# Kernel optimization log

Hardware: AMD Instinct MI355X
Metric: run time of the kernel (lower is better)

Reference implementation:

```python
import jax, jax.numpy as jnp
import numpy as np

N0, N1, N2, N3, B = 120000, 20000, 6000, 1600, 64
E1, E2, E3 = 480000, 144000, 38400
KS = 5  # kernel size per dim; K = 125 total


def spline_basis(pseudo, ks=KS):
    # open B-spline basis, degree 1, over [0,1]^3 (torch_spline_conv semantics)
    p = pseudo * (ks - 1)                       # (E,3)
    lo = jnp.clip(jnp.floor(p), 0.0, ks - 2.0)  # (E,3)
    f = p - lo                                  # fractional part
    bits = jnp.array([[(s >> d) & 1 for d in range(3)] for s in range(8)],
                     dtype=jnp.float32)         # (8,3) corner offsets
    w = jnp.where(bits[None] > 0, f[:, None, :], 1.0 - f[:, None, :])  # (E,8,3)
    basis = w[..., 0] * w[..., 1] * w[..., 2]   # (E,8)
    strides = jnp.array([1.0, ks, ks * ks], dtype=jnp.float32)
    kidx = ((lo[:, None, :] + bits[None]) * strides).sum(-1).astype(jnp.int32)  # (E,8)
    return basis, kidx


def spline_conv(x, edge_index, pseudo, W, root, bias, num_nodes):
    src, dst = edge_index[0], edge_index[1]
    basis, kidx = spline_basis(pseudo)                   # (E,8), (E,8)
    XW = jnp.einsum('ni,kio->nko', x, W)                 # (N,K,out)
    taps = XW[src[:, None], kidx]                        # (E,8,out) gather
    msg = (taps * basis[..., None]).sum(axis=1)          # (E,out)
    agg = jax.ops.segment_sum(msg, dst, num_segments=num_nodes)
    deg = jax.ops.segment_sum(jnp.ones_like(dst, jnp.float32), dst,
                              num_segments=num_nodes)
    agg = agg / jnp.maximum(deg, 1.0)[:, None]           # mean aggregation
    return agg + x @ root + bias


def seg_max(x, seg, n):
    v = jax.ops.segment_max(x, seg, num_segments=n)
    return jnp.where(jnp.isfinite(v), v, 0.0)  # empty voxels -> 0


def setup_inputs() -> dict:
    key = jax.random.key(0)
    ks = jax.random.split(key, 24)
    return {
        'x0': jax.random.uniform(ks[0], (N0, 1), jnp.float32),
        'cluster0': jax.random.randint(ks[1], (N0,), 0, N1),
        'edge1': jax.random.randint(ks[2], (2, E1), 0, N1),
        'pseudo1': jax.random.uniform(ks[3], (E1, 3), jnp.float32),
        'W1': jax.random.normal(ks[4], (125, 1, 64), jnp.float32) * 0.1,
        'root1': jax.random.normal(ks[5], (1, 64), jnp.float32) * 0.1,
        'b1': jnp.zeros((64,), jnp.float32),
        'cluster1': jax.random.randint(ks[6], (N1,), 0, N2),
        'edge2': jax.random.randint(ks[7], (2, E2), 0, N2),
        'pseudo2': jax.random.uniform(ks[8], (E2, 3), jnp.float32),
        'W2': jax.random.normal(ks[9], (125, 64, 64), jnp.float32) * 0.05,
        'root2': jax.random.normal(ks[10], (64, 64), jnp.float32) * 0.05,
        'b2': jnp.zeros((64,), jnp.float32),
        'cluster2': jax.random.randint(ks[11], (N2,), 0, N3),
        'edge3': jax.random.randint(ks[12], (2, E3), 0, N3),
        'pseudo3': jax.random.uniform(ks[13], (E3, 3), jnp.float32),
        'W3': jax.random.normal(ks[14], (125, 64, 128), jnp.float32) * 0.05,
        'root3': jax.random.normal(ks[15], (64, 128), jnp.float32) * 0.05,
        'b3': jnp.zeros((128,), jnp.float32),
        'cluster3': jax.random.randint(ks[16], (N3,), 0, B * 8),
        'fc1_w': jax.random.normal(ks[17], (1024, 256), jnp.float32) * 0.03,
        'fc1_b': jnp.zeros((256,), jnp.float32),
        'fc2_w': jax.random.normal(ks[18], (256, 10), jnp.float32) * 0.06,
        'fc2_b': jnp.zeros((10,), jnp.float32),
    }


def reference(x0, cluster0, edge1, pseudo1, W1, root1, b1,
              cluster1, edge2, pseudo2, W2, root2, b2,
              cluster2, edge3, pseudo3, W3, root3, b3,
              cluster3, fc1_w, fc1_b, fc2_w, fc2_b):
    x = seg_max(x0, cluster0, N1)                       # sparse voxel max pool 1
    x = jax.nn.elu(spline_conv(x, edge1, pseudo1, W1, root1, b1, N1))
    x = seg_max(x, cluster1, N2)                        # pool 2
    x = jax.nn.elu(spline_conv(x, edge2, pseudo2, W2, root2, b2, N2))
    x = seg_max(x, cluster2, N3)                        # pool 3
    x = jax.nn.elu(spline_conv(x, edge3, pseudo3, W3, root3, b3, N3))
    x = seg_max(x, cluster3, B * 8)                     # dense 2x2x2 voxel pool
    x = x.reshape(B, 8 * 128)
    x = jax.nn.elu(x @ fc1_w + fc1_b)
    x = x @ fc2_w + fc2_b
    return jax.nn.log_softmax(x, axis=1)
```

## Files before the change

### kernel.cpp

```cpp
#include <hip/hip_runtime.h>
#include <hip/hip_bf16.h>
#include <math.h>

#define N0c 120000
#define N1c 20000
#define N2c 6000
#define N3c 1600
#define E1c 480000
#define E2c 144000
#define E3c 38400

#define HB1 32
#define HB2 120
#define HB3 40
#define CVT2B 2000
#define CVT3B 4000
#define SS0B  469

typedef __attribute__((ext_vector_type(8))) short short8;
typedef __attribute__((ext_vector_type(4))) float f32x4;

__device__ __forceinline__ float eluf(float x) {
    return x > 0.0f ? x : expm1f(x);
}

__device__ __forceinline__ unsigned f2sort(float f) {
    unsigned u = __float_as_uint(f);
    return (u & 0x80000000u) ? ~u : (u | 0x80000000u);
}
__device__ __forceinline__ float sort2f(unsigned u) {
    unsigned bits = (u & 0x80000000u) ? (u & 0x7FFFFFFFu) : ~u;
    return __uint_as_float(bits);
}
__device__ __forceinline__ unsigned short f2bf(float v) {
    unsigned u = __float_as_uint(v);
    unsigned r = (u + 0x7FFFu + ((u >> 16) & 1u)) >> 16;
    return (unsigned short)r;
}

__global__ __launch_bounds__(256) void hist_all(
    const int* __restrict__ edge1, const int* __restrict__ edge2,
    const int* __restrict__ edge3,
    const float* __restrict__ pseudo2, const float* __restrict__ pseudo3,
    const float* __restrict__ W2, const float* __restrict__ W3,
    const float* __restrict__ x0, const int* __restrict__ cluster0,
    int* __restrict__ blockCnt1,
    int* __restrict__ blockCnt2, int* __restrict__ cntD2,
    int* __restrict__ blockCnt3, int* __restrict__ cntD3,
    unsigned short* __restrict__ W2t, unsigned short* __restrict__ W3t,
    unsigned* __restrict__ xm1)
{
    __shared__ int h[1250];
    int b = blockIdx.x, t = threadIdx.x;
    if (b < HB1) {
        for (int i = t; i < 1250; i += 256) h[i] = 0;
        __syncthreads();
        for (int e = b * 256 + t; e < E1c; e += HB1 * 256)
            atomicAdd(&h[edge1[E1c + e] >> 4], 1);
        __syncthreads();
        for (int i = t; i < 1250; i += 256) blockCnt1[i * HB1 + b] = h[i];
    } else if (b < HB1 + HB2 + HB3) {
        bool is2 = b < HB1 + HB2;
        int rb = is2 ? (b - HB1) : (b - HB1 - HB2);
        int nblk = is2 ? HB2 : HB3;
        int E = is2 ? E2c : E3c;
        const int* edge = is2 ? edge2 : edge3;
        const float* pseudo = is2 ? pseudo2 : pseudo3;
        int* blockCnt = is2 ? blockCnt2 : blockCnt3;
        int* dstCnt = is2 ? cntD2 : cntD3;
        int nb = is2 ? HB2 : HB3;
        if (t < 64) h[t] = 0;
        __syncthreads();
        for (int e = rb * 256 + t; e < E; e += nblk * 256) {
            int c = 0, mul = 1;
            #pragma unroll
            for (int d = 0; d < 3; d++) {
                float p = pseudo[e * 3 + d] * 4.0f;
                float l = fminf(fmaxf(floorf(p), 0.0f), 3.0f);
                c += (int)l * mul;
                mul <<= 2;
            }
            atomicAdd(&h[c], 1);
            atomicAdd(&dstCnt[edge[E + e]], 1);
        }
        __syncthreads();
        if (t < 64) blockCnt[t * nb + rb] = h[t];
    } else if (b < HB1 + HB2 + HB3 + CVT2B) {
        int idx = (b - (HB1 + HB2 + HB3)) * 256 + t;
        if (idx < 125 * 64 * 64) {
            int ic = idx & 63, kn = idx >> 6;
            int n = kn & 63, k = kn >> 6;
            W2t[idx] = f2bf(W2[((size_t)k * 64 + ic) * 64 + n]);
        }
    } else if (b < HB1 + HB2 + HB3 + CVT2B + CVT3B) {
        int idx = (b - (HB1 + HB2 + HB3 + CVT2B)) * 256 + t;
        if (idx < 125 * 128 * 64) {
            int ic = idx & 63, kn = idx >> 6;
            int n = kn & 127, k = kn >> 7;
            W3t[idx] = f2bf(W3[((size_t)k * 64 + ic) * 128 + n]);
        }
    } else {
        int idx = (b - (HB1 + HB2 + HB3 + CVT2B + CVT3B)) * 256 + t;
        if (idx < N0c)
            atomicMax(&xm1[cluster0[idx]], f2sort(x0[idx]));
    }
}

__global__ __launch_bounds__(256) void plan_tot(
    const int* __restrict__ blockCnt1, int* __restrict__ start1,
    const int* __restrict__ blockCnt2, int* __restrict__ binCnt2,
    int* __restrict__ binStart2, int* __restrict__ blkPrefix2,
    int* __restrict__ chunkBin2, int* __restrict__ chunkOff2,
    const int* __restrict__ blockCnt3, int* __restrict__ binCnt3,
    int* __restrict__ binStart3, int* __restrict__ blkPrefix3,
    int* __restrict__ chunkBin3, int* __restrict__ chunkOff3)
{
    __shared__ int ps[256];
    __shared__ int ps64[64];
    int t = threadIdx.x;

    int loc[5];
    int s = 0;
    #pragma unroll
    for (int i = 0; i < 5; i++) {
        int bin = t * 5 + i;
        int v = 0;
        if (bin < 1250) {
            const int4* row = (const int4*)(blockCnt1 + (size_t)bin * HB1);
            #pragma unroll
            for (int j = 0; j < HB1 / 4; j++) {
                int4 q = row[j];
                v += q.x + q.y + q.z + q.w;
            }
        }
        loc[i] = v;
        s += v;
    }
    ps[t] = s;
    __syncthreads();
    for (int ofs = 1; ofs < 256; ofs <<= 1) {
        int add = (t >= ofs) ? ps[t - ofs] : 0;
        __syncthreads();
        ps[t] += add;
        __syncthreads();
    }
    int run = (t == 0) ? 0 : ps[t - 1];
    #pragma unroll
    for (int i = 0; i < 5; i++) {
        int bin = t * 5 + i;
        if (bin < 1250) {
            start1[bin] = run;
            run += loc[i];
        }
    }
    if (t == 255) start1[1250] = run;
    __syncthreads();

    if (t < 64) {
        int v = 0;
        const int4* row = (const int4*)(blockCnt2 + (size_t)t * HB2);
        for (int j = 0; j < HB2 / 4; j++) {
            int4 q = row[j];
            v += q.x + q.y + q.z + q.w;
        }
        binCnt2[t] = v;
        ps64[t] = v;
    }
    __syncthreads();
    if (t == 0) {
        int s2 = 0, p = 0;
        for (int c = 0; c < 64; c++) {
            int v = ps64[c];
            binStart2[c] = s2;
            blkPrefix2[c] = p;
            s2 += v;
            p += (v + 63) >> 6;
        }
        binStart2[64] = s2;
        blkPrefix2[64] = p;
    }
    __syncthreads();
    if (t < 64) {
        int nch = (binCnt2[t] + 63) >> 6;
        int base = blkPrefix2[t];
        for (int j = 0; j < nch; j++) {
            chunkBin2[base + j] = t;
            chunkOff2[base + j] = j;
        }
    }
    __syncthreads();

    if (t < 64) {
        int v = 0;
        const int4* row = (const int4*)(blockCnt3 + (size_t)t * HB3);
        for (int j = 0; j < HB3 / 4; j++) {
            int4 q = row[j];
            v += q.x + q.y + q.z + q.w;
        }
        binCnt3[t] = v;
        ps64[t] = v;
    }
    __syncthreads();
    if (t == 0) {
        int s3 = 0, p = 0;
        for (int c = 0; c < 64; c++) {
            int v = ps64[c];
            binStart3[c] = s3;
            blkPrefix3[c] = p;
            s3 += v;
            p += (v + 63) >> 6;
        }
        binStart3[64] = s3;
        blkPrefix3[64] = p;
    }
    __syncthreads();
    if (t < 64) {
        int nch = (binCnt3[t] + 63) >> 6;
        int base = blkPrefix3[t];
        for (int j = 0; j < nch; j++) {
            chunkBin3[base + j] = t;
            chunkOff3[base + j] = j;
        }
    }
}

__global__ __launch_bounds__(256) void off_all(
    const int* __restrict__ blockCnt1, const int* __restrict__ start1,
    int* __restrict__ blockOff1,
    const int* __restrict__ blockCnt2, const int* __restrict__ binStart2,
    int* __restrict__ blockOff2,
    const int* __restrict__ blockCnt3, const int* __restrict__ binStart3,
    int* __restrict__ blockOff3)
{
    int r = blockIdx.x * 256 + threadIdx.x;
    if (r < 1250) {
        int run = start1[r];
        const int* c = blockCnt1 + (size_t)r * HB1;
        int* o = blockOff1 + (size_t)r * HB1;
        #pragma unroll 4
        for (int b = 0; b < HB1; b++) { o[b] = run; run += c[b]; }
    } else if (r < 1250 + 64) {
        int bin = r - 1250;
        int run = binStart2[bin];
        const int* c = blockCnt2 + (size_t)bin * HB2;
        int* o = blockOff2 + (size_t)bin * HB2;
        #pragma unroll 4
        for (int b = 0; b < HB2; b++) { o[b] = run; run += c[b]; }
    } else if (r < 1250 + 128) {
        int bin = r - 1314;
        int run = binStart3[bin];
        const int* c = blockCnt3 + (size_t)bin * HB3;
        int* o = blockOff3 + (size_t)bin * HB3;
        #pragma unroll 4
        for (int b = 0; b < HB3; b++) { o[b] = run; run += c[b]; }
    }
}

__global__ __launch_bounds__(256) void scatter_all(
    const int* __restrict__ edge1, const float* __restrict__ pseudo1,
    const int* __restrict__ edge2, const float* __restrict__ pseudo2,
    const int* __restrict__ edge3, const float* __restrict__ pseudo3,
    const int* __restrict__ blockOff1, const int* __restrict__ blockOff2,
    const int* __restrict__ blockOff3,
    int4* __restrict__ rec1, int4* __restrict__ rec2, int4* __restrict__ rec3,
    unsigned* __restrict__ xm1)
{
    __shared__ int cur[1250];
    int b = blockIdx.x, t = threadIdx.x;
    if (b < HB1) {
        for (int i = t; i < 1250; i += 256) cur[i] = blockOff1[(size_t)i * HB1 + b];
        __syncthreads();
        for (int e = b * 256 + t; e < E1c; e += HB1 * 256) {
            int src = edge1[e], dst = edge1[E1c + e];
            float f[3];
            int kbase = 0, mul5 = 1;
            #pragma unroll
            for (int d = 0; d < 3; d++) {
                float pp = pseudo1[e * 3 + d] * 4.0f;
                float l = fminf(fmaxf(floorf(pp), 0.0f), 3.0f);
                f[d] = pp - l;
                kbase += (int)l * mul5;
                mul5 *= 5;
            }
            int p = atomicAdd(&cur[dst >> 4], 1);
            rec1[p] = make_int4(src | ((dst & 15) << 16) | (kbase << 20),
                                __float_as_int(f[0]), __float_as_int(f[1]),
                                __float_as_int(f[2]));
        }
    } else if (b < HB1 + HB2 + HB3) {
        bool is2 = b < HB1 + HB2;
        int rb = is2 ? (b - HB1) : (b - HB1 - HB2);
        int nblk = is2 ? HB2 : HB3;
        int E = is2 ? E2c : E3c;
        const int* edge = is2 ? edge2 : edge3;
        const float* pseudo = is2 ? pseudo2 : pseudo3;
        const int* blockOff = is2 ? blockOff2 : blockOff3;
        int4* rec = is2 ? rec2 : rec3;
        int nb = is2 ? HB2 : HB3;
        if (t < 64) cur[t] = blockOff[(size_t)t * nb + rb];
        __syncthreads();
        for (int e = rb * 256 + t; e < E; e += nblk * 256) {
            int src = edge[e], dst = edge[E + e];
            float f[3];
            int c = 0, mul = 1;
            #pragma unroll
            for (int d = 0; d < 3; d++) {
                float pp = pseudo[e * 3 + d] * 4.0f;
                float l = fminf(fmaxf(floorf(pp), 0.0f), 3.0f);
                f[d] = pp - l;
                c += (int)l * mul;
                mul <<= 2;
            }
            int p = atomicAdd(&cur[c], 1);
            rec[p] = make_int4(src | (dst << 16),
                               __float_as_int(f[0]), __float_as_int(f[1]),
                               __float_as_int(f[2]));
        }
    } else {
        int idx = (b - (HB1 + HB2 + HB3)) * 256 + t;
        if (idx < N1c) {
            float f = sort2f(xm1[idx]);
            unsigned bb = __float_as_uint(f);
            if ((bb & 0x7F800000u) == 0x7F800000u) f = 0.0f;
            ((float*)xm1)[idx] = f;
        }
    }
}

__global__ __launch_bounds__(256) void conv1_block(
    const int4* __restrict__ rec, const float* __restrict__ x,
    const int* __restrict__ start,
    const float* __restrict__ W, const float* __restrict__ root,
    const float* __restrict__ bias, const int* __restrict__ cl,
    unsigned* __restrict__ xmOut) {
    __shared__ float T[16][128];
    __shared__ int degL[16];
    int b = blockIdx.x;
    for (int j = threadIdx.x; j < 2048; j += 256) ((float*)T)[j] = 0.0f;
    if (threadIdx.x < 16) degL[threadIdx.x] = 0;
    __syncthreads();
    int s0 = start[b], s1 = start[b + 1];
    for (int i = s0 + threadIdx.x; i < s1; i += 256) {
        int4 r = rec[i];
        int src = r.x & 0xFFFF;
        int ln = (r.x >> 16) & 15;
        int kbase = r.x >> 20;
        float f0 = __int_as_float(r.y);
        float f1 = __int_as_float(r.z);
        float f2 = __int_as_float(r.w);
        float xv = x[src];
        #pragma unroll
        for (int s = 0; s < 8; s++) {
            int b0 = s & 1, b1 = (s >> 1) & 1, b2 = (s >> 2) & 1;
            float w0 = b0 ? f0 : 1.0f - f0;
            float w1 = b1 ? f1 : 1.0f - f1;
            float w2 = b2 ? f2 : 1.0f - f2;
            int k = kbase + b0 + 5 * b1 + 25 * b2;
            atomicAdd(&T[ln][k], xv * w0 * w1 * w2);
        }
        atomicAdd(&degL[ln], 1);
    }
    __syncthreads();
    int w = threadIdx.x >> 6, lane = threadIdx.x & 63;
    float acc[4] = {0.0f, 0.0f, 0.0f, 0.0f};
    for (int k = 0; k < 125; k++) {
        float wv = W[(k << 6) + lane];
        #pragma unroll
        for (int j = 0; j < 4; j++)
            acc[j] = fmaf(T[w + 4 * j][k], wv, acc[j]);
    }
    int v0 = b << 4;
    #pragma unroll
    for (int j = 0; j < 4; j++) {
        int ln = w + 4 * j;
        int v = v0 + ln;
        float d = fmaxf((float)degL[ln], 1.0f);
        float val = eluf(acc[j] / d + x[v] * root[lane] + bias[lane]);
        atomicMax(&xmOut[((size_t)cl[v] << 6) + lane], f2sort(val));
    }
}

__global__ void decode_cvt(unsigned* __restrict__ buf,
                           unsigned short* __restrict__ xb, int total) {
    int idx = blockIdx.x * blockDim.x + threadIdx.x;
    if (idx >= total) return;
    float f = sort2f(buf[idx]);
    unsigned b = __float_as_uint(f);
    if ((b & 0x7F800000u) == 0x7F800000u) f = 0.0f;
    ((float*)buf)[idx] = f;
    xb[idx] = f2bf(f);
}

__global__ void segmax_decode(unsigned* __restrict__ buf, int total) {
    int idx = blockIdx.x * blockDim.x + threadIdx.x;
    if (idx >= total) return;
    float f = sort2f(buf[idx]);
    unsigned b = __float_as_uint(f);
    if ((b & 0x7F800000u) == 0x7F800000u) f = 0.0f;
    ((float*)buf)[idx] = f;
}

template<int COUT>
__global__ __launch_bounds__(256) void spline_mfma(
    const int4* __restrict__ recs,
    const unsigned short* __restrict__ Wt,
    const unsigned short* __restrict__ xb,
    const int* __restrict__ binStart,
    const int* __restrict__ binCnt,
    const int* __restrict__ blkPrefix,
    const int* __restrict__ chunkBin,
    const int* __restrict__ chunkOff,
    float* __restrict__ agg)
{
    __shared__ float basisS[4][8][64];
    __shared__ int srcS[4][64];
    __shared__ int dstS[4][64];

    int w = threadIdx.x >> 6, lane = threadIdx.x & 63;
    int c = blockIdx.x * 4 + w;
    if (c >= blkPrefix[64]) return;
    int bin = chunkBin[c];
    int chunk = chunkOff[c];
    int cnt = binCnt[bin];

    {
        int pos = chunk * 64 + lane;
        bool act = pos < cnt;
        int4 r = act ? recs[binStart[bin] + pos] : make_int4(0, 0, 0, 0);
        srcS[w][lane] = r.x & 0xFFFF;
        dstS[w][lane] = act ? (r.x >> 16) : -1;
        float f0 = __int_as_float(r.y);
        float f1 = __int_as_float(r.z);
        float f2 = __int_as_float(r.w);
        #pragma unroll
        for (int s = 0; s < 8; s++) {
            float w0 = (s & 1) ? f0 : 1.0f - f0;
            float w1 = (s & 2) ? f1 : 1.0f - f1;
            float w2 = (s & 4) ? f2 : 1.0f - f2;
            basisS[w][s][lane] = act ? (w0 * w1 * w2) : 0.0f;
        }
    }
    __builtin_amdgcn_wave_barrier();
    __threadfence_block();

    int lo0 = bin & 3, lo1 = (bin >> 2) & 3, lo2 = bin >> 4;
    int kbase = lo0 + 5 * lo1 + 25 * lo2;
    int colOff = (COUT == 128) ? (blockIdx.y << 6) : 0;
    int q = lane >> 4;
    int mcol = lane & 15;

    short8 afr[4][2];
    #pragma unroll
    for (int rt = 0; rt < 4; rt++) {
        int src = srcS[w][rt * 16 + mcol];
        const unsigned short* xr = xb + ((size_t)src << 6) + q * 8;
        afr[rt][0] = *(const short8*)(xr);
        afr[rt][1] = *(const short8*)(xr + 32);
    }

    f32x4 acc[4][4];
    #pragma unroll
    for (int rt = 0; rt < 4; rt++)
        #pragma unroll
        for (int nt = 0; nt < 4; nt++)
            acc[rt][nt] = (f32x4){0.0f, 0.0f, 0.0f, 0.0f};
    const f32x4 zero4 = {0.0f, 0.0f, 0.0f, 0.0f};

    #pragma unroll 1
    for (int s = 0; s < 8; s++) {
        int k = kbase + (s & 1) + 5 * ((s >> 1) & 1) + 25 * (s >> 2);
        const unsigned short* Wk = Wt + ((size_t)k * COUT + colOff) * 64;
        short8 bfr[4][2];
        #pragma unroll
        for (int nt = 0; nt < 4; nt++) {
            const unsigned short* Wn = Wk + (size_t)(nt * 16 + mcol) * 64 + q * 8;
            bfr[nt][0] = *(const short8*)(Wn);
            bfr[nt][1] = *(const short8*)(Wn + 32);
        }
        #pragma unroll
        for (int rt = 0; rt < 4; rt++) {
            f32x4 ct[4];
            #pragma unroll
            for (int nt = 0; nt < 4; nt++) {
                ct[nt] = __builtin_amdgcn_mfma_f32_16x16x32_bf16(afr[rt][0], bfr[nt][0], zero4, 0, 0, 0);
                ct[nt] = __builtin_amdgcn_mfma_f32_16x16x32_bf16(afr[rt][1], bfr[nt][1], ct[nt], 0, 0, 0);
            }
            #pragma unroll
            for (int r = 0; r < 4; r++) {
                float bs = basisS[w][s][rt * 16 + q * 4 + r];
                #pragma unroll
                for (int nt = 0; nt < 4; nt++)
                    acc[rt][nt][r] = fmaf(bs, ct[nt][r], acc[rt][nt][r]);
            }
        }
    }

    #pragma unroll
    for (int rt = 0; rt < 4; rt++) {
        #pragma unroll
        for (int r = 0; r < 4; r++) {
            int d = dstS[w][rt * 16 + q * 4 + r];
            if (d >= 0) {
                float* ap = agg + (size_t)d * COUT + colOff + mcol;
                #pragma unroll
                for (int nt = 0; nt < 4; nt++)
                    atomicAdd(ap + nt * 16, acc[rt][nt][r]);
            }
        }
    }
}

__global__ __launch_bounds__(256) void node_update64(
    const float* __restrict__ agg, const int* __restrict__ deg,
    const float* __restrict__ xm, const float* __restrict__ root,
    const float* __restrict__ bias, const int* __restrict__ cl,
    unsigned* __restrict__ xmOut, int nNodes) {
    __shared__ float xsh[4][64];
    int w = threadIdx.x >> 6, lane = threadIdx.x & 63;
    int v = blockIdx.x * 4 + w;
    if (v >= nNodes) return;
    xsh[w][lane] = xm[((size_t)v << 6) + lane];
    float a = agg[((size_t)v << 6) + lane] / fmaxf((float)deg[v], 1.0f);
    float r = 0.0f;
    #pragma unroll 8
    for (int i = 0; i < 64; i++)
        r = fmaf(xsh[w][i], root[(i << 6) + lane], r);
    float val = eluf(a + r + bias[lane]);
    atomicMax(&xmOut[((size_t)cl[v] << 6) + lane], f2sort(val));
}

__global__ __launch_bounds__(256) void node_update128(
    const float* __restrict__ agg, const int* __restrict__ deg,
    const float* __restrict__ xm, const float* __restrict__ root,
    const float* __restrict__ bias, const int* __restrict__ cl,
    unsigned* __restrict__ xmOut, int nNodes) {
    __shared__ float xsh[4][64];
    int w = threadIdx.x >> 6, lane = threadIdx.x & 63;
    int v = blockIdx.x * 4 + w;
    if (v >= nNodes) return;
    xsh[w][lane] = xm[((size_t)v << 6) + lane];
    float dinv = 1.0f / fmaxf((float)deg[v], 1.0f);
    float a0 = agg[((size_t)v << 7) + lane] * dinv;
    float a1 = agg[((size_t)v << 7) + 64 + lane] * dinv;
    float r0 = 0.0f, r1 = 0.0f;
    #pragma unroll 8
    for (int i = 0; i < 64; i++) {
        float xi = xsh[w][i];
        r0 = fmaf(xi, root[(i << 7) + lane], r0);
        r1 = fmaf(xi, root[(i << 7) + 64 + lane], r1);
    }
    unsigned* orow = xmOut + ((size_t)cl[v] << 7);
    atomicMax(&orow[lane], f2sort(eluf(a0 + r0 + bias[lane])));
    atomicMax(&orow[64 + lane], f2sort(eluf(a1 + r1 + bias[lane + 64])));
}

__global__ __launch_bounds__(256) void fc1_split(
    const float* __restrict__ xin, const float* __restrict__ w1,
    float* __restrict__ h) {
    __shared__ float xsh[128];
    int row = blockIdx.x, ks = blockIdx.y;
    int o = threadIdx.x;
    if (o < 128) xsh[o] = xin[row * 1024 + ks * 128 + o];
    __syncthreads();
    float acc = 0.0f;
    const float* wp = w1 + (size_t)ks * 128 * 256 + o;
    #pragma unroll 8
    for (int i = 0; i < 128; i++)
        acc = fmaf(xsh[i], wp[i * 256], acc);
    atomicAdd(&h[row * 256 + o], acc);
}

__global__ __launch_bounds__(64) void fc2_k(
    const float* __restrict__ h, const float* __restrict__ b1,
    const float* __restrict__ w2, const float* __restrict__ b2,
    float* __restrict__ out) {
    __shared__ float hs[256];
    __shared__ float lg[10];
    int row = blockIdx.x;
    int t = threadIdx.x;
    for (int i = t; i < 256; i += 64) hs[i] = eluf(h[row * 256 + i] + b1[i]);
    __syncthreads();
    if (t < 10) {
        float a = b2[t];
        for (int i = 0; i < 256; i++) a = fmaf(hs[i], w2[i * 10 + t], a);
        lg[t] = a;
    }
    __syncthreads();
    if (t < 10) {
        float m = -1e30f;
        #pragma unroll
        for (int j = 0; j < 10; j++) m = fmaxf(m, lg[j]);
        float sum = 0.0f;
        #pragma unroll
        for (int j = 0; j < 10; j++) sum += expf(lg[j] - m);
        out[row * 10 + t] = lg[t] - m - logf(sum);
    }
}

extern "C" void kernel_launch(void* const* d_in, const int* in_sizes, int n_in,
                              void* d_out, int out_size, void* d_ws, size_t ws_size,
                              hipStream_t stream) {
    const float* x0      = (const float*)d_in[0];
    const int*   cluster0= (const int*)d_in[1];
    const int*   edge1   = (const int*)d_in[2];
    const float* pseudo1 = (const float*)d_in[3];
    const float* W1      = (const float*)d_in[4];
    const float* root1   = (const float*)d_in[5];
    const float* b1      = (const float*)d_in[6];
    const int*   cluster1= (const int*)d_in[7];
    const int*   edge2   = (const int*)d_in[8];
    const float* pseudo2 = (const float*)d_in[9];
    const float* W2      = (const float*)d_in[10];
    const float* root2   = (const float*)d_in[11];
    const float* b2      = (const float*)d_in[12];
    const int*   cluster2= (const int*)d_in[13];
    const int*   edge3   = (const int*)d_in[14];
    const float* pseudo3 = (const float*)d_in[15];
    const float* W3      = (const float*)d_in[16];
    const float* root3   = (const float*)d_in[17];
    const float* b3      = (const float*)d_in[18];
    const int*   cluster3= (const int*)d_in[19];
    const float* fc1_w   = (const float*)d_in[20];
    const float* fc1_b   = (const float*)d_in[21];
    const float* fc2_w   = (const float*)d_in[22];
    const float* fc2_b   = (const float*)d_in[23];
    float* out = (float*)d_out;

    float* ws = (float*)d_ws;
    size_t off = 0;
    float* xm1  = ws + off; off += 20480;
    float* xm2  = ws + off; off += (size_t)N2c * 64;
    float* xm3  = ws + off; off += (size_t)N3c * 64;
    float* xm4  = ws + off; off += 512 * 128;
    float* agg2 = ws + off; off += (size_t)N2c * 64;
    float* agg3 = ws + off; off += (size_t)N3c * 128;
    float* h1   = ws + off; off += 64 * 256;
    int* cntD2   = (int*)(ws + off); off += 6016;
    int* cntD3   = (int*)(ws + off); off += 1664;
    size_t zeroFloats = off;
    int4* rec1 = (int4*)(ws + off); off += (size_t)E1c * 4;
    int4* rec2 = (int4*)(ws + off); off += (size_t)E2c * 4;
    int4* rec3 = (int4*)(ws + off); off += (size_t)E3c * 4;
    unsigned short* W2t = (unsigned short*)(ws + off); off += 256000;
    unsigned short* W3t = (unsigned short*)(ws + off); off += 512000;
    unsigned short* xb2 = (unsigned short*)(ws + off); off += 192000;
    unsigned short* xb3 = (unsigned short*)(ws + off); off += 51200;
    int* start1    = (int*)(ws + off); off += 1280;
    int* blockCnt1 = (int*)(ws + off); off += HB1 * 1250;
    int* blockOff1 = (int*)(ws + off); off += HB1 * 1250;
    int* blockCnt2 = (int*)(ws + off); off += HB2 * 64;
    int* blockOff2 = (int*)(ws + off); off += HB2 * 64;
    int* blockCnt3 = (int*)(ws + off); off += HB3 * 64;
    int* blockOff3 = (int*)(ws + off); off += HB3 * 64;
    int* binCnt2   = (int*)(ws + off); off += 64;
    int* binStart2 = (int*)(ws + off); off += 80;
    int* blkPrefix2= (int*)(ws + off); off += 80;
    int* chunkBin2 = (int*)(ws + off); off += 2560;
    int* chunkOff2 = (int*)(ws + off); off += 2560;
    int* binCnt3   = (int*)(ws + off); off += 64;
    int* binStart3 = (int*)(ws + off); off += 80;
    int* blkPrefix3= (int*)(ws + off); off += 80;
    int* chunkBin3 = (int*)(ws + off); off += 768;
    int* chunkOff3 = (int*)(ws + off); off += 768;

    hipMemsetAsync(d_ws, 0, zeroFloats * sizeof(float), stream);

    hist_all<<<HB1 + HB2 + HB3 + CVT2B + CVT3B + SS0B, 256, 0, stream>>>(
        edge1, edge2, edge3, pseudo2, pseudo3, W2, W3, x0, cluster0,
        blockCnt1, blockCnt2, cntD2, blockCnt3, cntD3,
        W2t, W3t, (unsigned*)xm1);

    plan_tot<<<1, 256, 0, stream>>>(
        blockCnt1, start1,
        blockCnt2, binCnt2, binStart2, blkPrefix2, chunkBin2, chunkOff2,
        blockCnt3, binCnt3, binStart3, blkPrefix3, chunkBin3, chunkOff3);

    off_all<<<6, 256, 0, stream>>>(
        blockCnt1, start1, blockOff1,
        blockCnt2, binStart2, blockOff2,
        blockCnt3, binStart3, blockOff3);

    scatter_all<<<HB1 + HB2 + HB3 + (N1c + 255) / 256, 256, 0, stream>>>(
        edge1, pseudo1, edge2, pseudo2, edge3, pseudo3,
        blockOff1, blockOff2, blockOff3, rec1, rec2, rec3, (unsigned*)xm1);

    conv1_block<<<1250, 256, 0, stream>>>(rec1, xm1, start1, W1, root1, b1,
                                          cluster1, (unsigned*)xm2);
    decode_cvt<<<(N2c * 64) / 256, 256, 0, stream>>>((unsigned*)xm2, xb2, N2c * 64);

    spline_mfma<64><<<dim3((E2c / 64 + 64 + 3) / 4, 1), 256, 0, stream>>>(
        rec2, W2t, xb2, binStart2, binCnt2, blkPrefix2, chunkBin2, chunkOff2, agg2);
    node_update64<<<(N2c + 3) / 4, 256, 0, stream>>>(agg2, cntD2, xm2, root2, b2,
                                                     cluster2, (unsigned*)xm3, N2c);
    decode_cvt<<<(N3c * 64) / 256, 256, 0, stream>>>((unsigned*)xm3, xb3, N3c * 64);

    spline_mfma<128><<<dim3((E3c / 64 + 64 + 3) / 4, 2), 256, 0, stream>>>(
        rec3, W3t, xb3, binStart3, binCnt3, blkPrefix3, chunkBin3, chunkOff3, agg3);
    node_update128<<<(N3c + 3) / 4, 256, 0, stream>>>(agg3, cntD3, xm3, root3, b3,
                                                      cluster3, (unsigned*)xm4, N3c);
    segmax_decode<<<(512 * 128) / 256, 256, 0, stream>>>((unsigned*)xm4, 512 * 128);

    fc1_split<<<dim3(64, 8), 256, 0, stream>>>(xm4, fc1_w, h1);
    fc2_k<<<64, 64, 0, stream>>>(h1, fc1_b, fc2_w, fc2_b, out);
}
```

Baseline: 350.5 us.

## Replace atomic scatter-add aggregation with per-edge messages and CSR gather

Layers 2 and 3 of the spline conv no longer atomically add each edge message into a per-node accumulator. The MFMA kernel writes dense per-edge messages, and the scatter pass builds a destination-sorted position list using a prefix sum over degrees computed in plan_tot. The node update kernels then gather and sum each node's messages deterministically. This removes float atomics and the zeroing of the aggregation buffers, at the cost of a larger message buffer (E2 x 64 floats), extra scatter atomics and posList writes, random reads in the gather, and a serial scan added to the single-block plan kernel.

New measurement: 349.9 us. No clear change (-0.2%).

```diff
diff --git a/kernel.cpp b/kernel.cpp
--- a/kernel.cpp
+++ b/kernel.cpp
@@ -113,7 +113,9 @@
     int* __restrict__ chunkBin2, int* __restrict__ chunkOff2,
     const int* __restrict__ blockCnt3, int* __restrict__ binCnt3,
     int* __restrict__ binStart3, int* __restrict__ blkPrefix3,
-    int* __restrict__ chunkBin3, int* __restrict__ chunkOff3)
+    int* __restrict__ chunkBin3, int* __restrict__ chunkOff3,
+    const int* __restrict__ cntD2, int* __restrict__ dstStart2,
+    const int* __restrict__ cntD3, int* __restrict__ dstStart3)
 {
     __shared__ int ps[256];
     __shared__ int ps64[64];
@@ -221,6 +223,62 @@
             chunkBin3[base + j] = t;
             chunkOff3[base + j] = j;
         }
+    }
+    __syncthreads();
+
+    {
+        int locd[24];
+        int sd = 0;
+        #pragma unroll
+        for (int i = 0; i < 24; i++) {
+            int bin = t * 24 + i;
+            int vv = (bin < N2c) ? cntD2[bin] : 0;
+            locd[i] = vv;
+            sd += vv;
+        }
+        ps[t] = sd;
+        __syncthreads();
+        for (int ofs = 1; ofs < 256; ofs <<= 1) {
+            int add = (t >= ofs) ? ps[t - ofs] : 0;
+            __syncthreads();
+            ps[t] += add;
+            __syncthreads();
+        }
+        int rund = (t == 0) ? 0 : ps[t - 1];
+        #pragma unroll
+        for (int i = 0; i < 24; i++) {
+            int bin = t * 24 + i;
+            if (bin < N2c) { dstStart2[bin] = rund; rund += locd[i]; }
+        }
+        if (t == 255) dstStart2[N2c] = ps[255];
+    }
+    __syncthreads();
+
+    {
+        int locd[7];
+        int sd = 0;
+        #pragma unroll
+        for (int i = 0; i < 7; i++) {
+            int bin = t * 7 + i;
+            int vv = (bin < N3c) ? cntD3[bin] : 0;
+            locd[i] = vv;
+            sd += vv;
+        }
+        ps[t] = sd;
+        __syncthreads();
+        for (int ofs = 1; ofs < 256; ofs <<= 1) {
+            int add = (t >= ofs) ? ps[t - ofs] : 0;
+            __syncthreads();
+            ps[t] += add;
+            __syncthreads();
+        }
+        int rund = (t == 0) ? 0 : ps[t - 1];
+        #pragma unroll
+        for (int i = 0; i < 7; i++) {
+            int bin = t * 7 + i;
+            if (bin < N3c) { dstStart3[bin] = rund; rund += locd[i]; }
+        }
+        if (t == 255) dstStart3[N3c] = ps[255];
     }
 }
 
@@ -263,7 +321,10 @@
     const int* __restrict__ blockOff1, const int* __restrict__ blockOff2,
     const int* __restrict__ blockOff3,
     int4* __restrict__ rec1, int4* __restrict__ rec2, int4* __restrict__ rec3,
-    unsigned* __restrict__ xm1)
+    unsigned* __restrict__ xm1,
+    const int* __restrict__ dstStart2, const int* __restrict__ dstStart3,
+    int* __restrict__ curD2, int* __restrict__ curD3,
+    int* __restrict__ posList2, int* __restrict__ posList3)
 {
     __shared__ int cur[1250];
     int b = blockIdx.x, t = threadIdx.x;
@@ -296,6 +357,9 @@
         const float* pseudo = is2 ? pseudo2 : pseudo3;
         const int* blockOff = is2 ? blockOff2 : blockOff3;
         int4* rec = is2 ? rec2 : rec3;
+        const int* dstStart = is2 ? dstStart2 : dstStart3;
+        int* curD = is2 ? curD2 : curD3;
+        int* posList = is2 ? posList2 : posList3;
         int nb = is2 ? HB2 : HB3;
         if (t < 64) cur[t] = blockOff[(size_t)t * nb + rb];
         __syncthreads();
@@ -315,6 +379,8 @@
             rec[p] = make_int4(src | (dst << 16),
                                __float_as_int(f[0]), __float_as_int(f[1]),
                                __float_as_int(f[2]));
+            int qd = dstStart[dst] + atomicAdd(&curD[dst], 1);
+            posList[qd] = p;
         }
     } else {
         int idx = (b - (HB1 + HB2 + HB3)) * 256 + t;
@@ -410,11 +476,10 @@
     const int* __restrict__ blkPrefix,
     const int* __restrict__ chunkBin,
     const int* __restrict__ chunkOff,
-    float* __restrict__ agg)
+    float* __restrict__ msg)
 {
     __shared__ float basisS[4][8][64];
     __shared__ int srcS[4][64];
-    __shared__ int dstS[4][64];
 
     int w = threadIdx.x >> 6, lane = threadIdx.x & 63;
     int c = blockIdx.x * 4 + w;
@@ -428,7 +493,6 @@
         bool act = pos < cnt;
         int4 r = act ? recs[binStart[bin] + pos] : make_int4(0, 0, 0, 0);
         srcS[w][lane] = r.x & 0xFFFF;
-        dstS[w][lane] = act ? (r.x >> 16) : -1;
         float f0 = __int_as_float(r.y);
         float f1 = __int_as_float(r.z);
         float f2 = __int_as_float(r.w);
@@ -495,23 +559,25 @@
         }
     }
 
+    int base = binStart[bin] + chunk * 64;
     #pragma unroll
     for (int rt = 0; rt < 4; rt++) {
         #pragma unroll
         for (int r = 0; r < 4; r++) {
-            int d = dstS[w][rt * 16 + q * 4 + r];
-            if (d >= 0) {
-                float* ap = agg + (size_t)d * COUT + colOff + mcol;
+            int row = rt * 16 + q * 4 + r;
+            if (chunk * 64 + row < cnt) {
+                float* mp = msg + (size_t)(base + row) * COUT + colOff + mcol;
                 #pragma unroll
                 for (int nt = 0; nt < 4; nt++)
-                    atomicAdd(ap + nt * 16, acc[rt][nt][r]);
+                    mp[nt * 16] = acc[rt][nt][r];
             }
         }
     }
 }
 
-__global__ __launch_bounds__(256) void node_update64(
-    const float* __restrict__ agg, const int* __restrict__ deg,
+__global__ __launch_bounds__(256) void agg_update64(
+    const float* __restrict__ msg, const int* __restrict__ posList,
+    const int* __restrict__ dstStart,
     const float* __restrict__ xm, const float* __restrict__ root,
     const float* __restrict__ bias, const int* __restrict__ cl,
     unsigned* __restrict__ xmOut, int nNodes) {
@@ -520,17 +586,31 @@
     int v = blockIdx.x * 4 + w;
     if (v >= nNodes) return;
     xsh[w][lane] = xm[((size_t)v << 6) + lane];
-    float a = agg[((size_t)v << 6) + lane] / fmaxf((float)deg[v], 1.0f);
+    int s0 = dstStart[v], s1 = dstStart[v + 1];
+    float a0 = 0.0f, a1 = 0.0f, a2 = 0.0f, a3 = 0.0f;
+    int i = s0;
+    for (; i + 4 <= s1; i += 4) {
+        int p0 = posList[i], p1 = posList[i + 1];
+        int p2 = posList[i + 2], p3 = posList[i + 3];
+        a0 += msg[((size_t)p0 << 6) + lane];
+        a1 += msg[((size_t)p1 << 6) + lane];
+        a2 += msg[((size_t)p2 << 6) + lane];
+        a3 += msg[((size_t)p3 << 6) + lane];
+    }
+    for (; i < s1; i++)
+        a0 += msg[((size_t)posList[i] << 6) + lane];
+    float a = (a0 + a1 + a2 + a3) / fmaxf((float)(s1 - s0), 1.0f);
     float r = 0.0f;
     #pragma unroll 8
-    for (int i = 0; i < 64; i++)
-        r = fmaf(xsh[w][i], root[(i << 6) + lane], r);
+    for (int j = 0; j < 64; j++)
+        r = fmaf(xsh[w][j], root[(j << 6) + lane], r);
     float val = eluf(a + r + bias[lane]);
     atomicMax(&xmOut[((size_t)cl[v] << 6) + lane], f2sort(val));
 }
 
-__global__ __launch_bounds__(256) void node_update128(
-    const float* __restrict__ agg, const int* __restrict__ deg,
+__global__ __launch_bounds__(256) void agg_update128(
+    const float* __restrict__ msg, const int* __restrict__ posList,
+    const int* __restrict__ dstStart,
     const float* __restrict__ xm, const float* __restrict__ root,
     const float* __restrict__ bias, const int* __restrict__ cl,
     unsigned* __restrict__ xmOut, int nNodes) {
@@ -539,19 +619,33 @@
     int v = blockIdx.x * 4 + w;
     if (v >= nNodes) return;
     xsh[w][lane] = xm[((size_t)v << 6) + lane];
-    float dinv = 1.0f / fmaxf((float)deg[v], 1.0f);
-    float a0 = agg[((size_t)v << 7) + lane] * dinv;
-    float a1 = agg[((size_t)v << 7) + 64 + lane] * dinv;
+    int s0 = dstStart[v], s1 = dstStart[v + 1];
+    float c0a = 0.0f, c0b = 0.0f, c1a = 0.0f, c1b = 0.0f;
+    int i = s0;
+    for (; i + 2 <= s1; i += 2) {
+        int p0 = posList[i], p1 = posList[i + 1];
+        const float* m0 = msg + ((size_t)p0 << 7);
+        const float* m1 = msg + ((size_t)p1 << 7);
+        c0a += m0[lane]; c0b += m0[64 + lane];
+        c1a += m1[lane]; c1b += m1[64 + lane];
+    }
+    for (; i < s1; i++) {
+        const float* m0 = msg + ((size_t)posList[i] << 7);
+        c0a += m0[lane]; c0b += m0[64 + lane];
+    }
+    float dinv = 1.0f / fmaxf((float)(s1 - s0), 1.0f);
+    float aa0 = (c0a + c1a) * dinv;
+    float aa1 = (c0b + c1b) * dinv;
     float r0 = 0.0f, r1 = 0.0f;
     #pragma unroll 8
-    for (int i = 0; i < 64; i++) {
-        float xi = xsh[w][i];
-        r0 = fmaf(xi, root[(i << 7) + lane], r0);
-        r1 = fmaf(xi, root[(i << 7) + 64 + lane], r1);
+    for (int j = 0; j < 64; j++) {
+        float xi = xsh[w][j];
+        r0 = fmaf(xi, root[(j << 7) + lane], r0);
+        r1 = fmaf(xi, root[(j << 7) + 64 + lane], r1);
     }
     unsigned* orow = xmOut + ((size_t)cl[v] << 7);
-    atomicMax(&orow[lane], f2sort(eluf(a0 + r0 + bias[lane])));
-    atomicMax(&orow[64 + lane], f2sort(eluf(a1 + r1 + bias[lane + 64])));
+    atomicMax(&orow[lane], f2sort(eluf(aa0 + r0 + bias[lane])));
+    atomicMax(&orow[64 + lane], f2sort(eluf(aa1 + r1 + bias[lane + 64])));
 }
 
 __global__ __launch_bounds__(256) void fc1_split(
@@ -632,11 +726,11 @@
     float* xm2  = ws + off; off += (size_t)N2c * 64;
     float* xm3  = ws + off; off += (size_t)N3c * 64;
     float* xm4  = ws + off; off += 512 * 128;
-    float* agg2 = ws + off; off += (size_t)N2c * 64;
-    float* agg3 = ws + off; off += (size_t)N3c * 128;
     float* h1   = ws + off; off += 64 * 256;
     int* cntD2   = (int*)(ws + off); off += 6016;
     int* cntD3   = (int*)(ws + off); off += 1664;
+    int* curD2   = (int*)(ws + off); off += 6016;
+    int* curD3   = (int*)(ws + off); off += 1664;
     size_t zeroFloats = off;
     int4* rec1 = (int4*)(ws + off); off += (size_t)E1c * 4;
     int4* rec2 = (int4*)(ws + off); off += (size_t)E2c * 4;
@@ -662,6 +756,11 @@
     int* blkPrefix3= (int*)(ws + off); off += 80;
     int* chunkBin3 = (int*)(ws + off); off += 768;
     int* chunkOff3 = (int*)(ws + off); off += 768;
+    int* dstStart2 = (int*)(ws + off); off += 6016;
+    int* dstStart3 = (int*)(ws + off); off += 1664;
+    int* posList2  = (int*)(ws + off); off += E2c;
+    int* posList3  = (int*)(ws + off); off += E3c;
+    float* msg = ws + off; off += (size_t)E2c * 64;
 
     hipMemsetAsync(d_ws, 0, zeroFloats * sizeof(float), stream);
 
@@ -673,7 +772,8 @@
     plan_tot<<<1, 256, 0, stream>>>(
         blockCnt1, start1,
         blockCnt2, binCnt2, binStart2, blkPrefix2, chunkBin2, chunkOff2,
-        blockCnt3, binCnt3, binStart3, blkPrefix3, chunkBin3, chunkOff3);
+        blockCnt3, binCnt3, binStart3, blkPrefix3, chunkBin3, chunkOff3,
+        cntD2, dstStart2, cntD3, dstStart3);
 
     off_all<<<6, 256, 0, stream>>>(
         blockCnt1, start1, blockOff1,
@@ -682,22 +782,25 @@
 
     scatter_all<<<HB1 + HB2 + HB3 + (N1c + 255) / 256, 256, 0, stream>>>(
         edge1, pseudo1, edge2, pseudo2, edge3, pseudo3,
-        blockOff1, blockOff2, blockOff3, rec1, rec2, rec3, (unsigned*)xm1);
+        blockOff1, blockOff2, blockOff3, rec1, rec2, rec3, (unsigned*)xm1,
+        dstStart2, dstStart3, curD2, curD3, posList2, posList3);
 
     conv1_block<<<1250, 256, 0, stream>>>(rec1, xm1, start1, W1, root1, b1,
                                           cluster1, (unsigned*)xm2);
     decode_cvt<<<(N2c * 64) / 256, 256, 0, stream>>>((unsigned*)xm2, xb2, N2c * 64);
 
     spline_mfma<64><<<dim3((E2c / 64 + 64 + 3) / 4, 1), 256, 0, stream>>>(
-        rec2, W2t, xb2, binStart2, binCnt2, blkPrefix2, chunkBin2, chunkOff2, agg2);
-    node_update64<<<(N2c + 3) / 4, 256, 0, stream>>>(agg2, cntD2, xm2, root2, b2,
-                                                     cluster2, (unsigned*)xm3, N2c);
+        rec2, W2t, xb2, binStart2, binCnt2, blkPrefix2, chunkBin2, chunkOff2, msg);
+    agg_update64<<<(N2c + 3) / 4, 256, 0, stream>>>(msg, posList2, dstStart2,
+                                                    xm2, root2, b2, cluster2,
+                                                    (unsigned*)xm3, N2c);
     decode_cvt<<<(N3c * 64) / 256, 256, 0, stream>>>((unsigned*)xm3, xb3, N3c * 64);
 
     spline_mfma<128><<<dim3((E3c / 64 + 64 + 3) / 4, 2), 256, 0, stream>>>(
-        rec3, W3t, xb3, binStart3, binCnt3, blkPrefix3, chunkBin3, chunkOff3, agg3);
-    node_update128<<<(N3c + 3) / 4, 256, 0, stream>>>(agg3, cntD3, xm3, root3, b3,
-                                                      cluster3, (unsigned*)xm4, N3c);
+        rec3, W3t, xb3, binStart3, binCnt3, blkPrefix3, chunkBin3, chunkOff3, msg);
+    agg_update128<<<(N3c + 3) / 4, 256, 0, stream>>>(msg, posList3, dstStart3,
+                                                     xm3, root3, b3, cluster3,
+                                                     (unsigned*)xm4, N3c);
     segmax_decode<<<(512 * 128) / 256, 256, 0, stream>>>((unsigned*)xm4, 512 * 128);
 
     fc1_split<<<dim3(64, 8), 256, 0, stream>>>(xm4, fc1_w, h1);
```
